# Optimization experiments

Measured on AMD Instinct MI355X. Metric: run time of the kernel, lower is better.

Reference implementation:

```python
import jax, jax.numpy as jnp
import numpy as np

B, C, N, K = 32, 1024, 2048, 64


def fps_indices(x, num):
    """Farthest-feature sampling. x: (B, N, C). Returns int32 indices (B, num).
    Deterministic start at index 0 (standard PointNet++ style loop)."""
    b, n, _ = x.shape

    def step(carry, _):
        dists, farthest = carry
        centroid = jnp.take_along_axis(x, farthest[:, None, None], axis=1)  # (B,1,C)
        d = jnp.sum((x - centroid) ** 2, axis=-1)  # (B,N)
        dists = jnp.minimum(dists, d)
        nxt = jnp.argmax(dists, axis=1).astype(jnp.int32)
        return (dists, nxt), farthest

    init = (jnp.full((b, n), 1e10, x.dtype), jnp.zeros((b,), jnp.int32))
    _, idx = jax.lax.scan(step, init, None, length=num)
    return idx.T  # (B, num)


def conv1x1(w, bias, x):
    # w: (out,in), x: (B,in,n) -> (B,out,n)
    return jnp.einsum('oi,bin->bon', w, x) + bias[:, None]


def setup_inputs() -> dict:
    key = jax.random.key(0)
    ks = jax.random.split(key, 16)
    s = 0.02
    return {
        'point_feat': jax.random.normal(ks[0], (B, C, N), jnp.float32),
        'global_feat': jax.random.normal(ks[1], (B, C), jnp.float32),
        'ps1_w': jax.random.normal(ks[2], (C, 128, K), jnp.float32) * s,
        'ps1_b': jnp.zeros((128,), jnp.float32),
        'm1c1_w': jax.random.normal(ks[3], (128, 2 * C + 128), jnp.float32) * s,
        'm1c1_b': jnp.zeros((128,), jnp.float32),
        'm1c2_w': jax.random.normal(ks[4], (128, 128), jnp.float32) * s,
        'm1c2_b': jnp.zeros((128,), jnp.float32),
        'm1sc_w': jax.random.normal(ks[5], (128, 2 * C + 128), jnp.float32) * s,
        'm1sc_b': jnp.zeros((128,), jnp.float32),
        'm2c1_w': jax.random.normal(ks[6], (64, 128), jnp.float32) * s,
        'm2c1_b': jnp.zeros((64,), jnp.float32),
        'm2c2_w': jax.random.normal(ks[7], (3, 64), jnp.float32) * s,
        'm2c2_b': jnp.zeros((3,), jnp.float32),
    }


def reference(point_feat, global_feat, ps1_w, ps1_b, m1c1_w, m1c1_b,
              m1c2_w, m1c2_b, m1sc_w, m1sc_b, m2c1_w, m2c1_b, m2c2_w, m2c2_b):
    # ffs: farthest-feature sample + gather
    xt = jnp.transpose(point_feat, (0, 2, 1))            # (B,N,C)
    idx = fps_indices(xt, K)                             # (B,K)
    feat_ffs = jnp.take_along_axis(xt, idx[:, :, None], axis=1)  # (B,K,C)
    feat_ffs = jnp.transpose(feat_ffs, (0, 2, 1))        # (B,C,K)

    # ConvTranspose1d on a length-1 input == outer product with kernel
    x1 = jnp.einsum('bi,iok->bok', global_feat, ps1_w) + ps1_b[:, None]  # (B,128,K)

    gf = jnp.broadcast_to(global_feat[:, :, None], (B, C, K))
    cat = jnp.concatenate([x1, feat_ffs, gf], axis=1)    # (B,2176,K)

    # MLP_Res
    shortcut = conv1x1(m1sc_w, m1sc_b, cat)
    h = conv1x1(m1c2_w, m1c2_b, jax.nn.relu(conv1x1(m1c1_w, m1c1_b, cat))) + shortcut

    # mlp_2
    pred = conv1x1(m2c2_w, m2c2_b, jax.nn.relu(conv1x1(m2c1_w, m2c1_b, h)))  # (B,3,K)
    return jnp.transpose(pred, (0, 2, 1))                # (B,K,3)
```

## Files before the change

kernel.cpp:

```cpp
#include <hip/hip_runtime.h>

#define BB_ 32
#define CC_ 1024
#define NN_ 2048
#define KK_ 64

typedef __bf16 bf16x8 __attribute__((ext_vector_type(8)));
typedef __bf16 bf16x2 __attribute__((ext_vector_type(2)));
typedef float f32x4 __attribute__((ext_vector_type(4)));
typedef unsigned int u32;

__device__ inline unsigned short f2bf_rn(float f) {
    unsigned u = __float_as_uint(f);
    unsigned r = (u + 0x7fffu + ((u >> 16) & 1u)) >> 16;
    return (unsigned short)r;
}

__device__ inline unsigned pack_bf16_rn(float f0, float f1) {
#if __has_builtin(__builtin_amdgcn_cvt_pk_bf16_f32)
    union { bf16x2 v; unsigned u; } x;
    x.v = __builtin_amdgcn_cvt_pk_bf16_f32(f0, f1);
    return x.u;
#else
    return (unsigned)f2bf_rn(f0) | ((unsigned)f2bf_rn(f1) << 16);
#endif
}

__device__ inline void split8(const float* f, uint4* H, uint4* L) {
    union { unsigned u[4]; uint4 v; } hq, lq;
#pragma unroll
    for (int j2 = 0; j2 < 4; j2++) {
        float a = f[2 * j2], c = f[2 * j2 + 1];
        unsigned hp = pack_bf16_rn(a, c);
        float h0f = __uint_as_float((hp & 0xffffu) << 16);
        float h1f = __uint_as_float(hp & 0xffff0000u);
        hq.u[j2] = hp;
        lq.u[j2] = pack_bf16_rn(a - h0f, c - h1f);
    }
    *H = hq.v; *L = lq.v;
}

__device__ inline void gload16(const void* g, void* l) {
    __builtin_amdgcn_global_load_lds(
        (const __attribute__((address_space(1))) u32*)g,
        (__attribute__((address_space(3))) u32*)l, 16, 0, 0);
}

__device__ void convert_body(const float* __restrict__ X,
                             unsigned char* __restrict__ Xc, int g0,
                             int cid, int t) {
    int chunk = cid & 7;
    int kt = (cid >> 3) & 31;
    int lb = cid >> 8;
    int n = chunk * 256 + t;
    int b = g0 + lb;
    const float* Xb = X + (size_t)b * CC_ * NN_;
    unsigned char* dst = Xc + (((size_t)lb * 32 + kt) * NN_ + n) * 128;
    int sw = n & 7;
#pragma unroll
    for (int q = 0; q < 4; q++) {
        float f[8];
#pragma unroll
        for (int j = 0; j < 8; j++)
            f[j] = Xb[(size_t)(kt * 32 + q * 8 + j) * NN_ + n];
        uint4 hq, lq;
        split8(f, &hq, &lq);
        int p = q ^ sw;
        *(uint4*)(dst + (p << 4)) = hq;
        *(uint4*)(dst + ((p ^ 4) << 4)) = lq;
    }
}

__global__ void convert_kernel(const float* __restrict__ X,
                               unsigned char* __restrict__ Xc, int g0) {
    convert_body(X, Xc, g0, blockIdx.x, threadIdx.x);
}

__device__ void fps_block(const float* Gb, int* idx, int b) {
    __shared__ float swv[2][4];
    __shared__ int swi[2][4];
    int t = threadIdx.x;
    float dist[8], nr[8];
#pragma unroll
    for (int r = 0; r < 8; r++) {
        nr[r] = Gb[(size_t)(t + 256 * r) * (NN_ + 1)];
        dist[r] = 1e10f;
    }
    if (t == 0) idx[b * KK_] = 0;
    int far = 0;
    for (int k = 1; k < KK_; k++) {
        float nf = Gb[(size_t)far * (NN_ + 1)];
        const float* grow = Gb + (size_t)far * NN_;
        float v = -1.f;
        int pi = 0;
#pragma unroll
        for (int r = 0; r < 8; r++) {
            float d = nr[r] + nf - 2.f * grow[t + 256 * r];
            dist[r] = fminf(dist[r], d);
            if (dist[r] > v) { v = dist[r]; pi = t + 256 * r; }
        }
#pragma unroll
        for (int off = 32; off; off >>= 1) {
            float ov = __shfl_down(v, off);
            int oi = __shfl_down(pi, off);
            if (ov > v || (ov == v && oi < pi)) { v = ov; pi = oi; }
        }
        int par = k & 1;
        if ((t & 63) == 0) { swv[par][t >> 6] = v; swi[par][t >> 6] = pi; }
        __syncthreads();
        float bv = swv[par][0];
        int bi = swi[par][0];
#pragma unroll
        for (int ww = 1; ww < 4; ww++) {
            float wv2 = swv[par][ww]; int wi2 = swi[par][ww];
            if (wv2 > bv || (wv2 == bv && wi2 < bi)) { bv = wv2; bi = wi2; }
        }
        far = bi;
        if (t == 0) idx[b * KK_ + k] = bi;
    }
}

__global__ __launch_bounds__(256, 2) void gram_fps_kernel(
    const unsigned char* __restrict__ Xc, float* __restrict__ G,
    const float* Gprev, int* __restrict__ idx, int nFps, int g0prev,
    const float* __restrict__ X, unsigned char* __restrict__ XcNext,
    int g0next, int nGram, int gs) {
    int bx = (int)blockIdx.x;
    if (bx < nFps) {
        fps_block(Gprev + (size_t)bx * NN_ * NN_, idx, g0prev + bx);
        return;
    }
    bx -= nFps;
    if (bx >= nGram) {
        convert_body(X, XcNext, g0next, bx - nGram, threadIdx.x);
        return;
    }
    int lb = bx % gs;
    int tt = bx / gs;
    int tn = (int)((sqrtf(8.f * tt + 1.f) - 1.f) * 0.5f);
    while ((tn + 1) * (tn + 2) / 2 <= tt) tn++;
    while (tn * (tn + 1) / 2 > tt) tn--;
    int tm = tt - tn * (tn + 1) / 2;
    bool diag = (tm == tn);
    int t = threadIdx.x;
    __shared__ __align__(16) unsigned char sMem[128 * 132 * 4];

    const unsigned char* XcB = Xc + (size_t)lb * 32 * NN_ * 128;
    int w = t >> 6, l = t & 63;
    int m0w = (w & 1) * 64, n0w = (w >> 1) * 64;
    int q = l >> 4, rr = l & 15;

    f32x4 zero = {0.f, 0.f, 0.f, 0.f};
    f32x4 acc[4][4];
#pragma unroll
    for (int mt = 0; mt < 4; mt++)
#pragma unroll
        for (int nt = 0; nt < 4; nt++) acc[mt][nt] = zero;

    auto stage = [&](int buf, int kt) {
        const unsigned char* Ab = XcB + ((size_t)kt * NN_ + (size_t)tm * 128) * 128;
        const unsigned char* Bb = XcB + ((size_t)kt * NN_ + (size_t)tn * 128) * 128;
        unsigned char* dA = sMem + buf * 32768;
        unsigned char* dB = dA + 16384;
#pragma unroll
        for (int r = 0; r < 4; r++) {
            gload16(Ab + r * 4096 + t * 16, dA + r * 4096 + t * 16);
            gload16(Bb + r * 4096 + t * 16, dB + r * 4096 + t * 16);
        }
    };

    stage(0, 0);
    for (int kt = 0; kt < 32; kt++) {
        int c = kt & 1;
        asm volatile("s_waitcnt vmcnt(0)" ::: "memory");
        __builtin_amdgcn_sched_barrier(0);
        __builtin_amdgcn_s_barrier();
        __builtin_amdgcn_sched_barrier(0);
        if (kt < 31) stage(c ^ 1, kt + 1);

        const unsigned char* cA = sMem + c * 32768;
        const unsigned char* cB = cA + 16384;
        bf16x8 ah[4], al[4], bh[4], bl[4];
#pragma unroll
        for (int mt = 0; mt < 4; mt++) {
            int ra = m0w + mt * 16 + rr;
            int pa = q ^ (ra & 7);
            ah[mt] = *(const bf16x8*)(cA + ra * 128 + (pa << 4));
            al[mt] = *(const bf16x8*)(cA + ra * 128 + ((pa ^ 4) << 4));
            int rb = n0w + mt * 16 + rr;
            int pb = q ^ (rb & 7);
            bh[mt] = *(const bf16x8*)(cB + rb * 128 + (pb << 4));
            bl[mt] = *(const bf16x8*)(cB + rb * 128 + ((pb ^ 4) << 4));
        }
#pragma unroll
        for (int mt = 0; mt < 4; mt++)
#pragma unroll
            for (int nt = 0; nt < 4; nt++) {
                acc[mt][nt] = __builtin_amdgcn_mfma_f32_16x16x32_bf16(ah[mt], bh[nt], acc[mt][nt], 0, 0, 0);
                acc[mt][nt] = __builtin_amdgcn_mfma_f32_16x16x32_bf16(ah[mt], bl[nt], acc[mt][nt], 0, 0, 0);
                acc[mt][nt] = __builtin_amdgcn_mfma_f32_16x16x32_bf16(al[mt], bh[nt], acc[mt][nt], 0, 0, 0);
            }
    }

    __syncthreads();
    float* Gb = G + (size_t)lb * NN_ * NN_;
    int i0 = tm * 128, j0 = tn * 128;
    int cc = l & 15;
    float* tb = (float*)sMem;
#pragma unroll
    for (int mt = 0; mt < 4; mt++)
#pragma unroll
        for (int nt = 0; nt < 4; nt++)
#pragma unroll
            for (int r = 0; r < 4; r++) {
                int gi = m0w + mt * 16 + q * 4 + r;
                int gj = n0w + nt * 16 + cc;
                float val = acc[mt][nt][r];
                Gb[(size_t)(i0 + gi) * NN_ + j0 + gj] = val;
                if (!diag) tb[gj * 132 + gi] = val;
            }
    if (!diag) {
        __syncthreads();
#pragma unroll
        for (int m = 0; m < 16; m++) {
            int f = t + 256 * m;
            int jj = f >> 5, sg = f & 31;
            float4 v4 = *(const float4*)(tb + jj * 132 + sg * 4);
            *(float4*)(&Gb[(size_t)(j0 + jj) * NN_ + i0 + sg * 4]) = v4;
        }
    }
}

__device__ void wconv_body(const float* __restrict__ w1, const float* __restrict__ wsc,
                           unsigned char* __restrict__ Wc, int it, int m) {
    const float* src = (m < 128 ? w1 + (size_t)m * 2176
                                : wsc + (size_t)(m - 128) * 2176) + it * 32;
    unsigned char* dst = Wc + ((size_t)it * 256 + m) * 128;
    int sw = m & 7;
#pragma unroll
    for (int q = 0; q < 4; q++) {
        float f[8];
        *(float4*)f       = *(const float4*)(src + q * 8);
        *(float4*)(f + 4) = *(const float4*)(src + q * 8 + 4);
        uint4 hq, lq;
        split8(f, &hq, &lq);
        int p = q ^ sw;
        *(uint4*)(dst + (p << 4)) = hq;
        *(uint4*)(dst + ((p ^ 4) << 4)) = lq;
    }
}

__device__ void catfillc_body(const float* __restrict__ X, const float* __restrict__ gf,
                              const int* __restrict__ idx,
                              unsigned char* __restrict__ Cc, int b, int cg, int t) {
    int k = t & 63;
    int chunk = cg * 4 + (t >> 6);
    int ch0 = 128 + chunk * 8;
    float f[8];
    if (ch0 < 1152) {
        int ik = idx[b * KK_ + k];
        const float* Xb = X + ((size_t)b * CC_ + (ch0 - 128)) * NN_ + ik;
#pragma unroll
        for (int j = 0; j < 8; j++) f[j] = Xb[(size_t)j * NN_];
    } else {
        const float* g = gf + (size_t)b * CC_ + (ch0 - 1152);
        *(float4*)f       = *(const float4*)g;
        *(float4*)(f + 4) = *(const float4*)(g + 4);
    }
    uint4 hq, lq;
    split8(f, &hq, &lq);
    int it = ch0 >> 5, q = (ch0 >> 3) & 3;
    unsigned char* dst = Cc + (((size_t)b * 68 + it) * 64 + k) * 128;
    int p = q ^ (k & 7);
    *(uint4*)(dst + (p << 4)) = hq;
    *(uint4*)(dst + ((p ^ 4) << 4)) = lq;
}

__device__ void cconv_body(const float* __restrict__ cat,
                           unsigned char* __restrict__ Cc, int it, int b, int t) {
    int k = t & 63, q = t >> 6;
    const float* src = cat + (size_t)b * 2176 * KK_ + (size_t)(it * 32 + q * 8) * KK_ + k;
    float f[8];
#pragma unroll
    for (int j = 0; j < 8; j++) f[j] = src[j * KK_];
    uint4 hq, lq;
    split8(f, &hq, &lq);
    unsigned char* dst = Cc + (((size_t)b * 68 + it) * 64 + k) * 128;
    int p = q ^ (k & 7);
    *(uint4*)(dst + (p << 4)) = hq;
    *(uint4*)(dst + ((p ^ 4) << 4)) = lq;
}

__global__ void x1_fps_kernel(const float* __restrict__ gf, const float* __restrict__ w,
                              const float* __restrict__ bias, float* __restrict__ cat,
                              const float* Gprev, int* __restrict__ idx,
                              int g0prev, int nFps, const float* __restrict__ X,
                              const float* __restrict__ w1, const float* __restrict__ wsc,
                              unsigned char* __restrict__ Wc,
                              unsigned char* __restrict__ Cc) {
    int bx = (int)blockIdx.x;
    int t = threadIdx.x;
    if (bx < nFps) {
        fps_block(Gprev + (size_t)bx * NN_ * NN_, idx, g0prev + bx);
        return;
    }
    bx -= nFps;
    if (bx < 128) {
        int okg = bx & 31, bg = bx >> 5;
        int ok = okg * 256 + t;
        int o = ok >> 6, k = ok & 63;
        float acc[8];
#pragma unroll
        for (int j = 0; j < 8; j++) acc[j] = 0.f;
        const float* g = gf + (size_t)(bg * 8) * CC_;
        for (int i = 0; i < CC_; i++) {
            float wv = w[(size_t)(i * 128 + o) * KK_ + k];
#pragma unroll
            for (int j = 0; j < 8; j++) acc[j] += g[j * CC_ + i] * wv;
        }
        float bv = bias[o];
#pragma unroll
        for (int j = 0; j < 8; j++)
            cat[((size_t)(bg * 8 + j) * 2176 + o) * KK_ + k] = acc[j] + bv;
        return;
    }
    bx -= 128;
    if (bx < 68) { wconv_body(w1, wsc, Wc, bx, t); return; }
    bx -= 68;
    catfillc_body(X, gf, idx, Cc, bx >> 6, bx & 63, t);
}

__global__ void tailconv_kernel(const float* __restrict__ cat, const float* __restrict__ X,
                                const float* __restrict__ gf, const int* __restrict__ idx,
                                unsigned char* __restrict__ Cc,
                                const float* __restrict__ w1, const float* __restrict__ wsc,
                                unsigned char* __restrict__ Wc, int nW, int catBase) {
    int bx = (int)blockIdx.x;
    int t = threadIdx.x;
    if (bx < 128) { cconv_body(cat, Cc, bx & 3, bx >> 2, t); return; }
    bx -= 128;
    if (bx < nW) { wconv_body(w1, wsc, Wc, bx, t); return; }
    bx -= nW;
    catfillc_body(X, gf, idx, Cc, catBase + (bx >> 6), bx & 63, t);
}

__global__ __launch_bounds__(256, 2) void mlp1m_kernel(
    const unsigned char* __restrict__ Wc, const unsigned char* __restrict__ Cc,
    float* __restrict__ P) {
    int s = blockIdx.x & 7, b = blockIdx.x >> 3;
    int nkt = (s < 4) ? 9 : 8;
    int kt0 = (s < 4) ? s * 9 : 36 + (s - 4) * 8;
    int t = threadIdx.x;
    __shared__ __align__(16) unsigned char sMem[2 * 40960];
    int w = t >> 6, l = t & 63;
    int m0w = w * 64;
    int q = l >> 4, rr = l & 15;
    const unsigned char* WcS = Wc + (size_t)kt0 * 32768;
    const unsigned char* CcS = Cc + ((size_t)b * 68 + kt0) * 8192;

    f32x4 zero = {0.f, 0.f, 0.f, 0.f};
    f32x4 acc[4][4];
#pragma unroll
    for (int mt = 0; mt < 4; mt++)
#pragma unroll
        for (int nt = 0; nt < 4; nt++) acc[mt][nt] = zero;

    auto stage = [&](int buf, int kt) {
        const unsigned char* A = WcS + (size_t)kt * 32768;
        const unsigned char* Bc = CcS + (size_t)kt * 8192;
        unsigned char* dA = sMem + buf * 40960;
        unsigned char* dB = dA + 32768;
#pragma unroll
        for (int r = 0; r < 8; r++)
            gload16(A + r * 4096 + t * 16, dA + r * 4096 + t * 16);
#pragma unroll
        for (int r = 0; r < 2; r++)
            gload16(Bc + r * 4096 + t * 16, dB + r * 4096 + t * 16);
    };

    stage(0, 0);
    for (int kt = 0; kt < nkt; kt++) {
        int c = kt & 1;
        asm volatile("s_waitcnt vmcnt(0)" ::: "memory");
        __builtin_amdgcn_sched_barrier(0);
        __builtin_amdgcn_s_barrier();
        __builtin_amdgcn_sched_barrier(0);
        if (kt < nkt - 1) stage(c ^ 1, kt + 1);

        const unsigned char* cA = sMem + c * 40960;
        const unsigned char* cB = cA + 32768;
        bf16x8 ah[4], al[4], bh[4], bl[4];
#pragma unroll
        for (int mt = 0; mt < 4; mt++) {
            int ra = m0w + mt * 16 + rr;
            int pa = q ^ (ra & 7);
            ah[mt] = *(const bf16x8*)(cA + ra * 128 + (pa << 4));
            al[mt] = *(const bf16x8*)(cA + ra * 128 + ((pa ^ 4) << 4));
            int rb = mt * 16 + rr;
            int pb = q ^ (rb & 7);
            bh[mt] = *(const bf16x8*)(cB + rb * 128 + (pb << 4));
            bl[mt] = *(const bf16x8*)(cB + rb * 128 + ((pb ^ 4) << 4));
        }
#pragma unroll
        for (int mt = 0; mt < 4; mt++)
#pragma unroll
            for (int nt = 0; nt < 4; nt++) {
                acc[mt][nt] = __builtin_amdgcn_mfma_f32_16x16x32_bf16(ah[mt], bh[nt], acc[mt][nt], 0, 0, 0);
                acc[mt][nt] = __builtin_amdgcn_mfma_f32_16x16x32_bf16(ah[mt], bl[nt], acc[mt][nt], 0, 0, 0);
                acc[mt][nt] = __builtin_amdgcn_mfma_f32_16x16x32_bf16(al[mt], bh[nt], acc[mt][nt], 0, 0, 0);
                acc[mt][nt] = __builtin_amdgcn_mfma_f32_16x16x32_bf16(al[mt], bl[nt], acc[mt][nt], 0, 0, 0);
            }
    }

    float* Pb = P + (size_t)(s * 32 + b) * 16384;
    int cc = l & 15;
#pragma unroll
    for (int mt = 0; mt < 4; mt++)
#pragma unroll
        for (int nt = 0; nt < 4; nt++)
#pragma unroll
            for (int r = 0; r < 4; r++) {
                int gi = m0w + mt * 16 + q * 4 + r;
                int gj = nt * 16 + cc;
                Pb[(size_t)gi * 64 + gj] = acc[mt][nt][r];
            }
}

__global__ void mlp2p_kernel(const float* __restrict__ P, const float* __restrict__ b1,
                             const float* __restrict__ bsc,
                             const float* __restrict__ w2, const float* __restrict__ b2,
                             const float* __restrict__ w3, const float* __restrict__ b3,
                             const float* __restrict__ w4, const float* __restrict__ b4,
                             float* __restrict__ out) {
    __shared__ float sT[128 * 32];
    __shared__ float sH[128 * 32];
    __shared__ float sR[64 * 32];
    const size_t SLAB = (size_t)32 * 256 * 64;
    int bx = blockIdx.x, t = threadIdx.x;
    int b = bx >> 1, k0 = (bx & 1) * 32;
    const float* Pb = P + (size_t)b * 16384;
    for (int j = t; j < 4096; j += 256) {
        int row = j >> 5, col = j & 31;
        const float* pp = Pb + (size_t)row * 64 + k0 + col;
        float s0 = 0.f;
#pragma unroll
        for (int s = 0; s < 8; s++) s0 += pp[s * SLAB];
        sT[row * 32 + col] = fmaxf(s0 + b1[row], 0.f);
    }
    __syncthreads();
    int k = t & 31, og = t >> 5;

#pragma unroll
    for (int pass = 0; pass < 2; pass++) {
        int o0 = og * 16 + pass * 8;
        float acc[8];
#pragma unroll
        for (int j = 0; j < 8; j++) {
            const float* pp = Pb + (size_t)(128 + o0 + j) * 64 + k0 + k;
            float s0 = 0.f;
#pragma unroll
            for (int s = 0; s < 8; s++) s0 += pp[s * SLAB];
            acc[j] = b2[o0 + j] + bsc[o0 + j] + s0;
        }
        for (int i4 = 0; i4 < 32; i4++) {
            float v0 = sT[(i4 * 4 + 0) * 32 + k];
            float v1 = sT[(i4 * 4 + 1) * 32 + k];
            float v2 = sT[(i4 * 4 + 2) * 32 + k];
            float v3 = sT[(i4 * 4 + 3) * 32 + k];
#pragma unroll
            for (int j = 0; j < 8; j++) {
                float4 wv = *(const float4*)(w2 + (size_t)(o0 + j) * 128 + i4 * 4);
                acc[j] += wv.x * v0 + wv.y * v1 + wv.z * v2 + wv.w * v3;
            }
        }
#pragma unroll
        for (int j = 0; j < 8; j++) sH[(o0 + j) * 32 + k] = acc[j];
    }
    __syncthreads();

    {
        int o0 = og * 8;
        float acc[8];
#pragma unroll
        for (int j = 0; j < 8; j++) acc[j] = b3[o0 + j];
        for (int i4 = 0; i4 < 32; i4++) {
            float v0 = sH[(i4 * 4 + 0) * 32 + k];
            float v1 = sH[(i4 * 4 + 1) * 32 + k];
            float v2 = sH[(i4 * 4 + 2) * 32 + k];
            float v3 = sH[(i4 * 4 + 3) * 32 + k];
#pragma unroll
            for (int j = 0; j < 8; j++) {
                float4 wv = *(const float4*)(w3 + (size_t)(o0 + j) * 128 + i4 * 4);
                acc[j] += wv.x * v0 + wv.y * v1 + wv.z * v2 + wv.w * v3;
            }
        }
#pragma unroll
        for (int j = 0; j < 8; j++) sR[(o0 + j) * 32 + k] = fmaxf(acc[j], 0.f);
    }
    __syncthreads();

    if (t < 96) {
        int o = t % 3;
        int kk = t / 3;
        float a0 = 0.f, a1 = 0.f, a2 = 0.f, a3 = 0.f;
        for (int i4 = 0; i4 < 16; i4++) {
            float4 wv = *(const float4*)(w4 + o * 64 + i4 * 4);
            a0 += wv.x * sR[(i4 * 4 + 0) * 32 + kk];
            a1 += wv.y * sR[(i4 * 4 + 1) * 32 + kk];
            a2 += wv.z * sR[(i4 * 4 + 2) * 32 + kk];
            a3 += wv.w * sR[(i4 * 4 + 3) * 32 + kk];
        }
        out[((size_t)b * KK_ + k0 + kk) * 3 + o] = b4[o] + ((a0 + a1) + (a2 + a3));
    }
}

__global__ void catfill_kernel(const float* __restrict__ X, const float* __restrict__ gf,
                               const int* __restrict__ idx, float* __restrict__ cat) {
    int b = blockIdx.y;
    int t = threadIdx.x;
    int ch = 128 + blockIdx.x * 4 + (t >> 6);
    int k = t & 63;
    float v;
    if (ch < 1152) {
        int c = ch - 128;
        int ik = idx[b * KK_ + k];
        v = X[((size_t)b * CC_ + c) * NN_ + ik];
    } else {
        v = gf[b * CC_ + (ch - 1152)];
    }
    cat[((size_t)b * 2176 + ch) * KK_ + k] = v;
}

__global__ void mlp1_kernel(const float* __restrict__ cat, const float* __restrict__ w1,
                            const float* __restrict__ b1, const float* __restrict__ wsc,
                            const float* __restrict__ bsc, float* __restrict__ t1,
                            float* __restrict__ sc) {
    __shared__ float red[2][16][64];
    int b = blockIdx.y, og = blockIdx.x;
    int t = threadIdx.x;
    int k = t & 63, sub = t >> 6;
    int o0 = og * 4;
    const float* cb = cat + (size_t)b * 2176 * KK_;
    float a1[4], a2[4];
#pragma unroll
    for (int j = 0; j < 4; j++) { a1[j] = 0.f; a2[j] = 0.f; }
    int iBeg = sub * 544;
    int off = (b & 7) * 68;
#pragma unroll 1
    for (int seg = 0; seg < 2; seg++) {
        int s0 = iBeg + (seg ? 0 : off);
        int s1 = seg ? iBeg + off : iBeg + 544;
        for (int i = s0; i < s1; i += 4) {
            float v0 = cb[(i + 0) * KK_ + k];
            float v1 = cb[(i + 1) * KK_ + k];
            float v2 = cb[(i + 2) * KK_ + k];
            float v3 = cb[(i + 3) * KK_ + k];
#pragma unroll
            for (int j = 0; j < 4; j++) {
                float4 wv = *(const float4*)(w1 + (size_t)(o0 + j) * 2176 + i);
                a1[j] += wv.x * v0 + wv.y * v1 + wv.z * v2 + wv.w * v3;
                float4 ws = *(const float4*)(wsc + (size_t)(o0 + j) * 2176 + i);
                a2[j] += ws.x * v0 + ws.y * v1 + ws.z * v2 + ws.w * v3;
            }
        }
    }
#pragma unroll
    for (int j = 0; j < 4; j++) {
        red[0][sub * 4 + j][k] = a1[j];
        red[1][sub * 4 + j][k] = a2[j];
    }
    __syncthreads();
#pragma unroll
    for (int p = t; p < 512; p += 256) {
        int m = p >> 8;
        int j = (p >> 6) & 3;
        int kk = p & 63;
        float s = red[m][j][kk] + red[m][4 + j][kk] + red[m][8 + j][kk] + red[m][12 + j][kk];
        int o = o0 + j;
        size_t oidx = ((size_t)b * 128 + o) * KK_ + kk;
        if (m == 0) t1[oidx] = fmaxf(s + b1[o], 0.f);
        else        sc[oidx] = s + bsc[o];
    }
}

__global__ void mlp2_kernel(const float* __restrict__ t1, const float* __restrict__ sc,
                            const float* __restrict__ w2, const float* __restrict__ b2,
                            const float* __restrict__ w3, const float* __restrict__ b3,
                            const float* __restrict__ w4, const float* __restrict__ b4,
                            float* __restrict__ out) {
    __shared__ float sT[128 * 32];
    __shared__ float sH[128 * 32];
    __shared__ float sR[64 * 32];
    int bx = blockIdx.x, t = threadIdx.x;
    int b = bx >> 1, k0 = (bx & 1) * 32;
    for (int j = t; j < 1024; j += 256) {
        int row = j >> 3, c4 = (j & 7) * 4;
        *(float4*)(sT + row * 32 + c4) =
            *(const float4*)(t1 + (size_t)b * 8192 + row * 64 + k0 + c4);
    }
    __syncthreads();
    int k = t & 31, og = t >> 5;
    const float* scb = sc + (size_t)b * 8192;

#pragma unroll
    for (int pass = 0; pass < 2; pass++) {
        int o0 = og * 16 + pass * 8;
        float acc[8];
#pragma unroll
        for (int j = 0; j < 8; j++) acc[j] = b2[o0 + j] + scb[(o0 + j) * 64 + k0 + k];
        for (int i4 = 0; i4 < 32; i4++) {
            float v0 = sT[(i4 * 4 + 0) * 32 + k];
            float v1 = sT[(i4 * 4 + 1) * 32 + k];
            float v2 = sT[(i4 * 4 + 2) * 32 + k];
            float v3 = sT[(i4 * 4 + 3) * 32 + k];
#pragma unroll
            for (int j = 0; j < 8; j++) {
                float4 wv = *(const float4*)(w2 + (size_t)(o0 + j) * 128 + i4 * 4);
                acc[j] += wv.x * v0 + wv.y * v1 + wv.z * v2 + wv.w * v3;
            }
        }
#pragma unroll
        for (int j = 0; j < 8; j++) sH[(o0 + j) * 32 + k] = acc[j];
    }
    __syncthreads();

    {
        int o0 = og * 8;
        float acc[8];
#pragma unroll
        for (int j = 0; j < 8; j++) acc[j] = b3[o0 + j];
        for (int i4 = 0; i4 < 32; i4++) {
            float v0 = sH[(i4 * 4 + 0) * 32 + k];
            float v1 = sH[(i4 * 4 + 1) * 32 + k];
            float v2 = sH[(i4 * 4 + 2) * 32 + k];
            float v3 = sH[(i4 * 4 + 3) * 32 + k];
#pragma unroll
            for (int j = 0; j < 8; j++) {
                float4 wv = *(const float4*)(w3 + (size_t)(o0 + j) * 128 + i4 * 4);
                acc[j] += wv.x * v0 + wv.y * v1 + wv.z * v2 + wv.w * v3;
            }
        }
#pragma unroll
        for (int j = 0; j < 8; j++) sR[(o0 + j) * 32 + k] = fmaxf(acc[j], 0.f);
    }
    __syncthreads();

    if (t < 96) {
        int o = t % 3;
        int kk = t / 3;
        float a0 = 0.f, a1 = 0.f, a2 = 0.f, a3 = 0.f;
        for (int i4 = 0; i4 < 16; i4++) {
            float4 wv = *(const float4*)(w4 + o * 64 + i4 * 4);
            a0 += wv.x * sR[(i4 * 4 + 0) * 32 + kk];
            a1 += wv.y * sR[(i4 * 4 + 1) * 32 + kk];
            a2 += wv.z * sR[(i4 * 4 + 2) * 32 + kk];
            a3 += wv.w * sR[(i4 * 4 + 3) * 32 + kk];
        }
        out[((size_t)b * KK_ + k0 + kk) * 3 + o] = b4[o] + ((a0 + a1) + (a2 + a3));
    }
}

extern "C" void kernel_launch(void* const* d_in, const int* in_sizes, int n_in,
                              void* d_out, int out_size, void* d_ws, size_t ws_size,
                              hipStream_t stream) {
    const float* X    = (const float*)d_in[0];
    const float* gf   = (const float*)d_in[1];
    const float* ps1w = (const float*)d_in[2];
    const float* ps1b = (const float*)d_in[3];
    const float* w1   = (const float*)d_in[4];
    const float* b1   = (const float*)d_in[5];
    const float* w2   = (const float*)d_in[6];
    const float* b2   = (const float*)d_in[7];
    const float* wsc  = (const float*)d_in[8];
    const float* bscp = (const float*)d_in[9];
    const float* w3   = (const float*)d_in[10];
    const float* b3   = (const float*)d_in[11];
    const float* w4   = (const float*)d_in[12];
    const float* b4   = (const float*)d_in[13];
    float* out = (float*)d_out;

    const size_t G_PER  = (size_t)NN_ * NN_ * 4;
    const size_t XC_PER = (size_t)32 * NN_ * 128;
    const size_t IDX_B  = (size_t)BB_ * KK_ * 4;
    const size_t CAT_B  = (size_t)BB_ * 2176 * KK_ * 4;
    const size_t T1_B   = (size_t)BB_ * 128 * KK_ * 4;
    size_t rest = IDX_B + CAT_B + 2 * T1_B;

    int gs = 1, merged = 0, pipe = 0;
    {
        const int tg[8]  = {8, 8, 4, 4, 2, 2, 1, 1};
        const int tmg[8] = {1, 1, 1, 1, 1, 1, 1, 0};
        const int tp[8]  = {1, 0, 1, 0, 1, 0, 0, 0};
        for (int i = 0; i < 8; i++) {
            size_t need = (size_t)(tmg[i] ? 2 : 1) * tg[i] * G_PER
                        + (size_t)(tp[i] ? 2 : 1) * tg[i] * XC_PER + rest;
            if (ws_size >= need) { gs = tg[i]; merged = tmg[i]; pipe = tp[i]; break; }
        }
    }

    char* ws = (char*)d_ws;
    float* Gbuf = (float*)ws;
    size_t gBufBytes = (size_t)(merged ? 2 : 1) * gs * G_PER;
    unsigned char* Xc0 = (unsigned char*)(ws + gBufBytes);
    unsigned char* Xc1 = Xc0 + (pipe ? (size_t)gs * XC_PER : 0);
    size_t xcBytes = (size_t)(pipe ? 2 : 1) * gs * XC_PER;
    char* p = (char*)Xc0 + xcBytes;
    int* idxws = (int*)p;    p += IDX_B;
    float* cat = (float*)p;  p += CAT_B;
    float* t1  = (float*)p;  p += T1_B;
    float* sc  = (float*)p;

    const size_t WC_B = (size_t)68 * 256 * 128;
    const size_t CC_B = (size_t)BB_ * 68 * 64 * 128;
    const size_t P_B  = (size_t)8 * BB_ * 256 * 64 * 4;
    char* scratch = nullptr;
    int inXc = 0;
    if (xcBytes >= WC_B + CC_B + P_B) { scratch = (char*)Xc0; inXc = 1; }
    else if (gBufBytes >= WC_B + CC_B + P_B) scratch = (char*)Gbuf;
    unsigned char* Wc = scratch ? (unsigned char*)scratch : nullptr;
    unsigned char* Cc = scratch ? Wc + WC_B : nullptr;
    float* P = scratch ? (float*)(Cc + CC_B) : nullptr;

    int ng = BB_ / gs;
    size_t halfElems = (size_t)gs * NN_ * NN_;
    int nGram = gs * 136;
    int nConvAll = 256 * gs;

    if (pipe) convert_kernel<<<nConvAll, 256, 0, stream>>>(X, Xc0, 0);
    for (int g = 0; g < ng; g++) {
        int g0 = g * gs;
        unsigned char* Xcur  = (g & 1) ? Xc1 : Xc0;
        unsigned char* Xnext = (g & 1) ? Xc0 : Xc1;
        if (!pipe) {
            Xcur = Xc0;
            convert_kernel<<<nConvAll, 256, 0, stream>>>(X, Xc0, g0);
        }
        float* Gcur = Gbuf + (merged ? (size_t)(g & 1) * halfElems : 0);
        float* Gprev = Gbuf + (merged ? (size_t)((g & 1) ^ 1) * halfElems : 0);
        int nFps = (merged && g > 0) ? gs : 0;
        int nConv = (pipe && g < ng - 1) ? nConvAll : 0;
        gram_fps_kernel<<<nFps + nGram + nConv, 256, 0, stream>>>(
            Xcur, Gcur, Gprev, idxws, nFps, g0 - gs, X, Xnext, g0 + gs, nGram, gs);
        if (!merged) {
            gram_fps_kernel<<<gs, 256, 0, stream>>>(
                Xcur, Gcur, Gcur, idxws, gs, g0, X, Xnext, 0, 0, gs);
        }
    }
    int nFpsLast = merged ? gs : 0;
    float* Glast = Gbuf + (merged ? (size_t)((ng - 1) & 1) * halfElems : 0);
    int nExtra = (scratch && inXc) ? 68 + (BB_ - gs) * 64 : 0;
    x1_fps_kernel<<<nFpsLast + 128 + nExtra, 256, 0, stream>>>(
        gf, ps1w, ps1b, cat, Glast, idxws, BB_ - gs, nFpsLast,
        X, w1, wsc, Wc, Cc);
    if (scratch) {
        int nW = inXc ? 0 : 68;
        int catBase = inXc ? BB_ - gs : 0;
        int nCat = inXc ? gs : BB_;
        tailconv_kernel<<<128 + nW + nCat * 64, 256, 0, stream>>>(
            cat, X, gf, idxws, Cc, w1, wsc, Wc, nW, catBase);
        mlp1m_kernel<<<256, 256, 0, stream>>>(Wc, Cc, P);
        mlp2p_kernel<<<BB_ * 2, 256, 0, stream>>>(P, b1, bscp, w2, b2, w3, b3, w4, b4, out);
    } else {
        catfill_kernel<<<dim3(512, BB_), 256, 0, stream>>>(X, gf, idxws, cat);
        mlp1_kernel<<<dim3(32, BB_), 256, 0, stream>>>(cat, w1, b1, wsc, bscp, t1, sc);
        mlp2_kernel<<<BB_ * 2, 256, 0, stream>>>(t1, sc, w2, b2, w3, b3, w4, b4, out);
    }
}
```

Before: 1.124 ms.

## Load Gram-matrix MFMA operands directly from global memory, dropping LDS staging

The bf16 Gram kernel no longer double-buffers A/B tiles through shared memory with async global-to-LDS loads and per-iteration barriers. Each wave now reads its MFMA fragments straight from global memory using precomputed swizzled offsets. This removes the barrier and LDS traffic, but it loses cross-wave reuse: each tile row is fetched by two waves, which relies on L2/L1 caching. It also exposes global load latency inside the MFMA loop because there is no prefetch.

```diff
diff --git a/kernel.cpp b/kernel.cpp
--- a/kernel.cpp
+++ b/kernel.cpp
@@ -150,6 +150,17 @@
     int m0w = (w & 1) * 64, n0w = (w >> 1) * 64;
     int q = l >> 4, rr = l & 15;
 
+    int offA[4], offB[4];
+#pragma unroll
+    for (int mt = 0; mt < 4; mt++) {
+        int ra = m0w + mt * 16 + rr;
+        offA[mt] = ra * 128 + ((q ^ (ra & 7)) << 4);
+        int rb = n0w + mt * 16 + rr;
+        offB[mt] = rb * 128 + ((q ^ (rb & 7)) << 4);
+    }
+    const unsigned char* Abase = XcB + (size_t)tm * 128 * 128;
+    const unsigned char* Bbase = XcB + (size_t)tn * 128 * 128;
+
     f32x4 zero = {0.f, 0.f, 0.f, 0.f};
     f32x4 acc[4][4];
 #pragma unroll
@@ -157,40 +168,16 @@
 #pragma unroll
         for (int nt = 0; nt < 4; nt++) acc[mt][nt] = zero;
 
-    auto stage = [&](int buf, int kt) {
-        const unsigned char* Ab = XcB + ((size_t)kt * NN_ + (size_t)tm * 128) * 128;
-        const unsigned char* Bb = XcB + ((size_t)kt * NN_ + (size_t)tn * 128) * 128;
-        unsigned char* dA = sMem + buf * 32768;
-        unsigned char* dB = dA + 16384;
-#pragma unroll
-        for (int r = 0; r < 4; r++) {
-            gload16(Ab + r * 4096 + t * 16, dA + r * 4096 + t * 16);
-            gload16(Bb + r * 4096 + t * 16, dB + r * 4096 + t * 16);
-        }
-    };
-
-    stage(0, 0);
     for (int kt = 0; kt < 32; kt++) {
-        int c = kt & 1;
-        asm volatile("s_waitcnt vmcnt(0)" ::: "memory");
-        __builtin_amdgcn_sched_barrier(0);
-        __builtin_amdgcn_s_barrier();
-        __builtin_amdgcn_sched_barrier(0);
-        if (kt < 31) stage(c ^ 1, kt + 1);
-
-        const unsigned char* cA = sMem + c * 32768;
-        const unsigned char* cB = cA + 16384;
+        const unsigned char* Ak = Abase + (size_t)kt * (NN_ * 128);
+        const unsigned char* Bk = Bbase + (size_t)kt * (NN_ * 128);
         bf16x8 ah[4], al[4], bh[4], bl[4];
 #pragma unroll
         for (int mt = 0; mt < 4; mt++) {
-            int ra = m0w + mt * 16 + rr;
-            int pa = q ^ (ra & 7);
-            ah[mt] = *(const bf16x8*)(cA + ra * 128 + (pa << 4));
-            al[mt] = *(const bf16x8*)(cA + ra * 128 + ((pa ^ 4) << 4));
-            int rb = n0w + mt * 16 + rr;
-            int pb = q ^ (rb & 7);
-            bh[mt] = *(const bf16x8*)(cB + rb * 128 + (pb << 4));
-            bl[mt] = *(const bf16x8*)(cB + rb * 128 + ((pb ^ 4) << 4));
+            ah[mt] = *(const bf16x8*)(Ak + offA[mt]);
+            al[mt] = *(const bf16x8*)(Ak + (offA[mt] ^ 64));
+            bh[mt] = *(const bf16x8*)(Bk + offB[mt]);
+            bl[mt] = *(const bf16x8*)(Bk + (offB[mt] ^ 64));
         }
 #pragma unroll
         for (int mt = 0; mt < 4; mt++)
```

New measurement: 1.278 ms. +13.7%, slower.
